# Kernel tuning notes

Hardware: AMD Instinct MI355X
Metric: run time of the kernel (lower is better)

Reference implementation:

```python
import jax, jax.numpy as jnp
import numpy as np

D_MODEL = 1024
NUM_HEADS = 16
HEAD_DIM = D_MODEL // NUM_HEADS
ROPE_THETA = 10000.0


def apply_rope(x, pos):
    # x: [B, H, S, Dh]; pos: [S] int. Interleaved-pair rotary embedding.
    d = x.shape[-1]
    inv_freq = 1.0 / (ROPE_THETA ** (jnp.arange(0, d, 2, dtype=jnp.float32) / d))  # [Dh/2]
    ang = pos.astype(jnp.float32)[:, None] * inv_freq[None, :]  # [S, Dh/2]
    cos, sin = jnp.cos(ang), jnp.sin(ang)
    x1 = x[..., 0::2]
    x2 = x[..., 1::2]
    r1 = x1 * cos - x2 * sin
    r2 = x1 * sin + x2 * cos
    return jnp.stack([r1, r2], axis=-1).reshape(x.shape)


def setup_inputs() -> dict:
    key = jax.random.key(0)
    ks = jax.random.split(key, 5)
    B, S = 4, 2048
    x = jax.random.normal(ks[0], (B, S, D_MODEL), dtype=jnp.float32)
    token_positions = jnp.arange(S, dtype=jnp.int32)
    scale = 1.0 / np.sqrt(D_MODEL)
    wq = jax.random.normal(ks[1], (D_MODEL, D_MODEL), dtype=jnp.float32) * scale
    wk = jax.random.normal(ks[2], (D_MODEL, D_MODEL), dtype=jnp.float32) * scale
    wv = jax.random.normal(ks[3], (D_MODEL, D_MODEL), dtype=jnp.float32) * scale
    wo = jax.random.normal(ks[4], (D_MODEL, D_MODEL), dtype=jnp.float32) * scale
    return {"x": x, "token_positions": token_positions, "wq": wq, "wk": wk, "wv": wv, "wo": wo}


def reference(x, token_positions, wq, wk, wv, wo):
    B, S, D = x.shape
    # Linear: einsum('d_out d_in, ... d_in -> ... d_out')
    def proj(w, t):
        return jnp.einsum('oi,bsi->bso', w, t)
    q = proj(wq, x).reshape(B, S, NUM_HEADS, HEAD_DIM).transpose(0, 2, 1, 3)  # [B,H,S,Dh]
    k = proj(wk, x).reshape(B, S, NUM_HEADS, HEAD_DIM).transpose(0, 2, 1, 3)
    v = proj(wv, x).reshape(B, S, NUM_HEADS, HEAD_DIM).transpose(0, 2, 1, 3)
    q = apply_rope(q, token_positions)
    k = apply_rope(k, token_positions)
    scores = jnp.einsum('bhqd,bhkd->bhqk', q, k) / jnp.sqrt(jnp.float32(HEAD_DIM))
    causal = jnp.tril(jnp.ones((S, S), dtype=bool))  # True = keep
    scores = jnp.where(causal, scores, -jnp.inf)
    attn = jax.nn.softmax(scores, axis=-1)
    out = jnp.einsum('bhqk,bhkd->bhqd', attn, v)  # [B,H,S,Dh]
    out = out.transpose(0, 2, 1, 3).reshape(B, S, D)
    return jnp.einsum('oi,bsi->bso', wo, out)
```

## Files before the change

### kernel.cpp

```cpp
#include <hip/hip_runtime.h>
#include <hip/hip_fp16.h>

#define DM   1024
#define NH   16
#define HD   64
#define BATCH 4
#define SEQ  2048
#define MROWS (BATCH*SEQ)
#define BHSD  ((size_t)BATCH*NH*SEQ*HD)

using f32x4 = __attribute__((ext_vector_type(4))) float;
using f16x8 = __attribute__((ext_vector_type(8))) _Float16;
using f16x4 = __attribute__((ext_vector_type(4))) _Float16;
using fp16x2 = __attribute__((ext_vector_type(2))) __fp16;
using u32x2 = __attribute__((ext_vector_type(2))) unsigned int;

__device__ __forceinline__ void gload_lds16(const void* g, void* l) {
    __builtin_amdgcn_global_load_lds(
        (const __attribute__((address_space(1))) void*)g,
        (__attribute__((address_space(3))) void*)l, 16, 0, 0);
}

__device__ __forceinline__ float red16_max(float v) {
    u32x2 r = __builtin_amdgcn_permlane16_swap(__float_as_uint(v), __float_as_uint(v), false, false);
    return fmaxf(__uint_as_float(r[0]), __uint_as_float(r[1]));
}
__device__ __forceinline__ float red32_max(float v) {
    u32x2 r = __builtin_amdgcn_permlane32_swap(__float_as_uint(v), __float_as_uint(v), false, false);
    return fmaxf(__uint_as_float(r[0]), __uint_as_float(r[1]));
}
__device__ __forceinline__ float red16_add(float v) {
    u32x2 r = __builtin_amdgcn_permlane16_swap(__float_as_uint(v), __float_as_uint(v), false, false);
    return __uint_as_float(r[0]) + __uint_as_float(r[1]);
}
__device__ __forceinline__ float red32_add(float v) {
    u32x2 r = __builtin_amdgcn_permlane32_swap(__float_as_uint(v), __float_as_uint(v), false, false);
    return __uint_as_float(r[0]) + __uint_as_float(r[1]);
}

__global__ __launch_bounds__(256) void f32_to_f16(const float* __restrict__ in,
                                                  _Float16* __restrict__ out, int n) {
    int i = (blockIdx.x * 256 + threadIdx.x) * 4;
    if (i >= n) return;
    float4 v = *(const float4*)(in + i);
    union { _Float16 h[4]; ushort4 u; } cv;
    cv.h[0] = (_Float16)v.x; cv.h[1] = (_Float16)v.y;
    cv.h[2] = (_Float16)v.z; cv.h[3] = (_Float16)v.w;
    *(ushort4*)(out + i) = cv.u;
}

__global__ __launch_bounds__(256) void rope_table(const int* __restrict__ pos,
                                                  float2* __restrict__ tab) {
    int idx = blockIdx.x * 256 + threadIdx.x;
    int s = idx >> 5, j = idx & 31;
    float p = (float)pos[s];
    float invf = powf(10000.0f, -(float)j / 32.0f);
    float ang = p * invf;
    tab[idx] = make_float2(cosf(ang), sinf(ang));
}

template<int MODE>
__global__ __launch_bounds__(256, 2)
void gemmT(const _Float16* __restrict__ A, const _Float16* __restrict__ Bw,
           float* __restrict__ outF, _Float16* __restrict__ qkv,
           const float2* __restrict__ rope) {
    constexpr int NK = DM / 32;
    __shared__ __align__(16) _Float16 ldsA[2][256][32];
    __shared__ __align__(16) _Float16 ldsB[2][128][32];
    const int tid  = threadIdx.x;
    const int lane = tid & 63;
    const int wid  = tid >> 6;
    const int m0 = blockIdx.x * 256;
    const int n0 = blockIdx.y * 128;
    const int wm = (wid >> 1) * 128;
    const int wn = (wid & 1) * 64;
    const int g   = lane >> 4;
    const int r16 = lane & 15;

    const _Float16* srcA[4];
    int dstA[4];
    #pragma unroll
    for (int L = 0; L < 4; ++L) {
        const int u = L*256 + tid, row = u >> 2, c = (u & 3) ^ ((row >> 1) & 3);
        srcA[L] = A + (size_t)(m0 + row)*DM + c*8;
        dstA[L] = u*8;
    }
    const _Float16* srcB[2];
    int dstB[2];
    #pragma unroll
    for (int L = 0; L < 2; ++L) {
        const int u = L*256 + tid, row = u >> 2, c = (u & 3) ^ ((row >> 1) & 3);
        srcB[L] = Bw + (size_t)(n0 + row)*DM + c*8;
        dstB[L] = u*8;
    }

    #define STAGE(buf, kt) do {                                        \
        const int ko = (kt)*32;                                        \
        _Float16* bA = &ldsA[(buf)][0][0];                             \
        _Float16* bB = &ldsB[(buf)][0][0];                             \
        gload_lds16(srcA[0] + ko, bA + dstA[0]);                       \
        gload_lds16(srcA[1] + ko, bA + dstA[1]);                       \
        gload_lds16(srcA[2] + ko, bA + dstA[2]);                       \
        gload_lds16(srcA[3] + ko, bA + dstA[3]);                       \
        gload_lds16(srcB[0] + ko, bB + dstB[0]);                       \
        gload_lds16(srcB[1] + ko, bB + dstB[1]);                       \
    } while (0)

    f32x4 acc[8][4] = {};

    STAGE(0, 0);
    for (int kt = 0; kt < NK; ++kt) {
        __syncthreads();
        if (kt + 1 < NK) STAGE((kt + 1) & 1, kt + 1);
        const int buf = kt & 1;
        f16x8 af[8], bf[4];
        #pragma unroll
        for (int i = 0; i < 8; ++i) {
            int row = wm + i*16 + r16;
            af[i] = *(const f16x8*)&ldsA[buf][row][(g ^ ((row >> 1) & 3)) * 8];
        }
        #pragma unroll
        for (int j = 0; j < 4; ++j) {
            int row = wn + j*16 + r16;
            bf[j] = *(const f16x8*)&ldsB[buf][row][(g ^ ((row >> 1) & 3)) * 8];
        }
        __builtin_amdgcn_s_setprio(1);
        #pragma unroll
        for (int i = 0; i < 8; ++i)
            #pragma unroll
            for (int j = 0; j < 4; ++j)
                acc[i][j] = __builtin_amdgcn_mfma_f32_16x16x32_f16(af[i], bf[j], acc[i][j], 0, 0, 0);
        __builtin_amdgcn_s_setprio(0);
    }
    #undef STAGE

    #pragma unroll
    for (int i = 0; i < 8; ++i) {
        #pragma unroll
        for (int j = 0; j < 4; ++j) {
            if constexpr (MODE == 0) {
                #pragma unroll
                for (int r = 0; r < 4; ++r) {
                    const int m = m0 + wm + i*16 + g*4 + r;
                    const int n = n0 + wn + j*16 + r16;
                    outF[(size_t)m*DM + n] = acc[i][j][r];
                }
            } else {
                const int n = n0 + wn + j*16 + r16;
                const int sel = n >> 10;
                const int cc = n & 1023;
                const int h = cc >> 6, dd = cc & 63;
                if (sel == 2) {
                    const int mb = m0 + wm + i*16 + g*4;
                    const int s0 = mb & (SEQ - 1), b = mb >> 11;
                    f16x4 pk;
                    #pragma unroll
                    for (int r = 0; r < 4; ++r) pk[r] = (_Float16)acc[i][j][r];
                    *(f16x4*)(qkv + 2*BHSD + ((size_t)((b*NH + h)*HD + dd))*SEQ + s0) = pk;
                } else {
                    #pragma unroll
                    for (int r = 0; r < 4; ++r) {
                        const int m = m0 + wm + i*16 + g*4 + r;
                        float v = acc[i][j][r];
                        float vp = __shfl_xor(v, 1);
                        const int s = m & (SEQ - 1), b = m >> 11;
                        float2 cs = rope[(s << 5) + (dd >> 1)];
                        float o;
                        if (dd & 1) o = vp * cs.y + v * cs.x;
                        else        o = v * cs.x - vp * cs.y;
                        if (sel == 0) o *= 0.18033688f;
                        qkv[(size_t)sel*BHSD + ((size_t)((b*NH + h)*SEQ + s))*HD + dd] = (_Float16)o;
                    }
                }
            }
        }
    }
}

__device__ __forceinline__ void process_tile(
    const _Float16 (*__restrict__ Klb)[64], const _Float16 (*__restrict__ Vlb)[64],
    const f16x8 (&qf)[2], f32x4 (&ot)[4], float &m, float &l,
    const int Rq, const int kv0, const int g, const int r16) {

    f32x4 sT[4] = {};
    const int kchunkBase = r16 & 7;
    __builtin_amdgcn_s_setprio(1);
    #pragma unroll
    for (int ks = 0; ks < 2; ++ks) {
        #pragma unroll
        for (int n = 0; n < 4; ++n) {
            f16x8 kf = *(const f16x8*)&Klb[n*16 + r16][(((ks<<2)|g) ^ kchunkBase)*8];
            sT[n] = __builtin_amdgcn_mfma_f32_16x16x32_f16(kf, qf[ks], sT[n], 0, 0, 0);
        }
    }
    __builtin_amdgcn_s_setprio(0);

    const bool full = (kv0 + 63 <= Rq);
    float sv[16];
    if (full) {
        #pragma unroll
        for (int n = 0; n < 4; ++n)
            #pragma unroll
            for (int r = 0; r < 4; ++r) sv[n*4 + r] = sT[n][r];
    } else {
        const int q = Rq + r16;
        #pragma unroll
        for (int n = 0; n < 4; ++n)
            #pragma unroll
            for (int r = 0; r < 4; ++r)
                sv[n*4 + r] = (kv0 + n*16 + 4*g + r <= q) ? sT[n][r] : -INFINITY;
    }
    float mx = sv[0];
    #pragma unroll
    for (int i = 1; i < 16; ++i) mx = fmaxf(mx, sv[i]);
    mx = red32_max(red16_max(mx));
    const bool need = (mx > m + 8.f);
    if (__any(need)) {
        float mnew = need ? mx : m;
        float al = exp2f(m - mnew);
        m = mnew;
        l *= al;
        #pragma unroll
        for (int n = 0; n < 4; ++n) ot[n] *= al;
    }
    float ps = 0.f;
    #pragma unroll
    for (int i = 0; i < 16; ++i) { sv[i] = exp2f(sv[i] - m); ps += sv[i]; }
    l += red32_add(red16_add(ps));

    uint pk[4][2];
    #pragma unroll
    for (int t = 0; t < 4; ++t)
        #pragma unroll
        for (int rp = 0; rp < 2; ++rp) {
            union { fp16x2 h; uint u; } cv;
            cv.h = __builtin_amdgcn_cvt_pkrtz(sv[t*4 + 2*rp], sv[t*4 + 2*rp + 1]);
            pk[t][rp] = cv.u;
        }
    uint w[2][4];
    #pragma unroll
    for (int kk = 0; kk < 2; ++kk)
        #pragma unroll
        for (int rp = 0; rp < 2; ++rp) {
            u32x2 s32 = __builtin_amdgcn_permlane32_swap(pk[2*kk][rp], pk[2*kk + 1][rp], false, false);
            u32x2 s16 = __builtin_amdgcn_permlane16_swap(s32[0], s32[1], false, false);
            w[kk][rp]     = s16[0];
            w[kk][2 + rp] = s16[1];
        }

    __builtin_amdgcn_s_setprio(1);
    #pragma unroll
    for (int ks = 0; ks < 2; ++ks) {
        union { uint u[4]; f16x8 h; } pb;
        #pragma unroll
        for (int j2 = 0; j2 < 4; ++j2) pb.u[j2] = w[ks][j2];
        #pragma unroll
        for (int n = 0; n < 4; ++n) {
            f16x8 vf = *(const f16x8*)&Vlb[n*16 + r16][(((ks<<2)|g) ^ kchunkBase)*8];
            ot[n] = __builtin_amdgcn_mfma_f32_16x16x32_f16(vf, pb.h, ot[n], 0, 0, 0);
        }
    }
    __builtin_amdgcn_s_setprio(0);
}

__global__ __launch_bounds__(256, 4)
void attn_kernel(const _Float16* __restrict__ qkv, _Float16* __restrict__ ao) {
    const int tid = threadIdx.x, lane = tid & 63, w = tid >> 6;
    const int g = lane >> 4, r16 = lane & 15;
    const int bh = blockIdx.x;
    const int jq = blockIdx.y;
    const int q0h = (31 - jq) * 64, q0l = jq * 64;
    const _Float16* Q   = qkv + (size_t)bh * SEQ * HD;
    const _Float16* Kp  = qkv + BHSD + (size_t)bh * SEQ * HD;
    const _Float16* Vpt = qkv + 2*BHSD + (size_t)bh * SEQ * HD;

    __shared__ __align__(16) _Float16 Kl[2][64][64];
    __shared__ __align__(16) _Float16 Vl[2][64][64];

    const int rA = tid >> 3,        rB = 32 + (tid >> 3);
    const int lcA = (tid & 7) ^ (rA & 7), lcB = (tid & 7) ^ (rB & 7);
    const _Float16* KsrcA = Kp  + (size_t)rA*HD + lcA*8;
    const _Float16* KsrcB = Kp  + (size_t)rB*HD + lcB*8;
    const _Float16* VsrcA = Vpt + (size_t)rA*SEQ + lcA*8;
    const _Float16* VsrcB = Vpt + (size_t)rB*SEQ + lcB*8;

    const int Rh = q0h + w*16, Rl = q0l + w*16;
    f16x8 qfh[2], qfl[2];
    #pragma unroll
    for (int ks = 0; ks < 2; ++ks) {
        qfh[ks] = *(const f16x8*)(Q + (size_t)(Rh + r16)*HD + ks*32 + g*8);
        qfl[ks] = *(const f16x8*)(Q + (size_t)(Rl + r16)*HD + ks*32 + g*8);
    }

    f32x4 oth[4] = {}, otl[4] = {};
    float mh = -INFINITY, lh = 0.f, ml_ = -INFINITY, ll_ = 0.f;

    const int nth = (q0h >> 6) + 1;
    const int ntl = (q0l >> 6) + 1;

    #define STAGE(buf, kv0) do {                                              \
        gload_lds16(KsrcA + (size_t)(kv0)*HD, &Kl[(buf)][0][0] + tid*8);      \
        gload_lds16(KsrcB + (size_t)(kv0)*HD, &Kl[(buf)][0][0] + (256+tid)*8);\
        gload_lds16(VsrcA + (kv0),            &Vl[(buf)][0][0] + tid*8);      \
        gload_lds16(VsrcB + (kv0),            &Vl[(buf)][0][0] + (256+tid)*8);\
    } while (0)

    STAGE(0, 0);
    for (int kt = 0; kt < nth; ++kt) {
        const int kv0 = kt << 6;
        __syncthreads();
        if (kt + 1 < nth) STAGE((kt + 1) & 1, (kt + 1) << 6);
        const int buf = kt & 1;

        if (kv0 <= Rh + 15)
            process_tile(Kl[buf], Vl[buf], qfh, oth, mh, lh, Rh, kv0, g, r16);
        if (kt < ntl)
            process_tile(Kl[buf], Vl[buf], qfl, otl, ml_, ll_, Rl, kv0, g, r16);
    }
    #undef STAGE

    const int b = bh >> 4, h = bh & 15;
    const float invh = 1.0f / lh, invl = 1.0f / ll_;
    _Float16* dsth = ao + ((size_t)(b*SEQ + Rh + r16))*DM + h*HD + g*4;
    _Float16* dstl = ao + ((size_t)(b*SEQ + Rl + r16))*DM + h*HD + g*4;
    #pragma unroll
    for (int n = 0; n < 4; ++n) {
        f16x4 pkh, pkl;
        #pragma unroll
        for (int r = 0; r < 4; ++r) {
            pkh[r] = (_Float16)(oth[n][r] * invh);
            pkl[r] = (_Float16)(otl[n][r] * invl);
        }
        *(f16x4*)(dsth + n*16) = pkh;
        *(f16x4*)(dstl + n*16) = pkl;
    }
}

extern "C" void kernel_launch(void* const* d_in, const int* in_sizes, int n_in,
                              void* d_out, int out_size, void* d_ws, size_t ws_size,
                              hipStream_t stream) {
    const float* x  = (const float*)d_in[0];
    const int*   tp = (const int*)d_in[1];
    const float* wq = (const float*)d_in[2];
    const float* wk = (const float*)d_in[3];
    const float* wv = (const float*)d_in[4];
    const float* wo = (const float*)d_in[5];
    float* out = (float*)d_out;

    char* ws = (char*)d_ws;
    _Float16* xh  = (_Float16*)(ws);
    _Float16* whq = (_Float16*)(ws + 16777216);
    _Float16* woh = (_Float16*)(ws + 23068672);
    _Float16* qkv = (_Float16*)(ws + 25165824);
    _Float16* ao  = (_Float16*)(ws + 75497472);
    float2*   rope= (float2*)  (ws + 92274688);

    f32_to_f16<<<MROWS*DM/1024, 256, 0, stream>>>(x, xh, MROWS*DM);
    f32_to_f16<<<DM*DM/1024, 256, 0, stream>>>(wq, whq,            DM*DM);
    f32_to_f16<<<DM*DM/1024, 256, 0, stream>>>(wk, whq + DM*DM,    DM*DM);
    f32_to_f16<<<DM*DM/1024, 256, 0, stream>>>(wv, whq + 2*DM*DM,  DM*DM);
    f32_to_f16<<<DM*DM/1024, 256, 0, stream>>>(wo, woh,            DM*DM);
    rope_table<<<SEQ*32/256, 256, 0, stream>>>(tp, rope);

    gemmT<1><<<dim3(MROWS/256, 3*DM/128), 256, 0, stream>>>(xh, whq, nullptr, qkv, rope);
    attn_kernel<<<dim3(BATCH*NH, 16), 256, 0, stream>>>(qkv, ao);
    gemmT<0><<<dim3(MROWS/256, DM/128), 256, 0, stream>>>(ao, woh, out, nullptr, nullptr);
}
```

Before: 215.9 us.

## Restructure projection GEMMs with 512-thread blocks, triple-buffered LDS and grid swizzle

Replaces the double-buffered 256-thread GEMM with a 512-thread, 8-wave kernel that prefetches three K-tiles ahead. Waits use explicit vmcnt counts and raw barriers instead of __syncthreads. The QKV projection now uses 256x256 tiles, and block indices are remapped so neighbouring blocks share A/B tiles in L2. This aims to hide global-load latency better and raise data reuse, at the cost of more LDS per block (one block per CU) and fragile hand-counted waitcnt logic.

```diff
diff --git a/kernel.cpp b/kernel.cpp
--- a/kernel.cpp
+++ b/kernel.cpp
@@ -60,36 +60,45 @@
 }
 
 template<int MODE>
-__global__ __launch_bounds__(256, 2)
-void gemmT(const _Float16* __restrict__ A, const _Float16* __restrict__ Bw,
+__global__ __launch_bounds__(512, 1)
+void gemmP(const _Float16* __restrict__ A, const _Float16* __restrict__ Bw,
            float* __restrict__ outF, _Float16* __restrict__ qkv,
            const float2* __restrict__ rope) {
     constexpr int NK = DM / 32;
-    __shared__ __align__(16) _Float16 ldsA[2][256][32];
-    __shared__ __align__(16) _Float16 ldsB[2][128][32];
+    constexpr int BN = MODE ? 256 : 128;
+    constexpr int WTM = MODE ? 8 : 4;
+    constexpr int BL = MODE ? 2 : 1;
+    __shared__ __align__(16) _Float16 ldsA[3][256][32];
+    __shared__ __align__(16) _Float16 ldsB[3][BN][32];
+
     const int tid  = threadIdx.x;
     const int lane = tid & 63;
     const int wid  = tid >> 6;
-    const int m0 = blockIdx.x * 256;
-    const int n0 = blockIdx.y * 128;
-    const int wm = (wid >> 1) * 128;
-    const int wn = (wid & 1) * 64;
+
+    const int nwg  = gridDim.x * gridDim.y;
+    const int flat = blockIdx.y * gridDim.x + blockIdx.x;
+    const int swz  = (flat % 8) * (nwg >> 3) + (flat >> 3);
+    const int m0 = (swz % gridDim.x) * 256;
+    const int n0 = (swz / gridDim.x) * BN;
+
+    const int wm = MODE ? ((wid >> 2) * 128) : ((wid >> 1) * 64);
+    const int wn = MODE ? ((wid & 3) * 64)   : ((wid & 1) * 64);
     const int g   = lane >> 4;
     const int r16 = lane & 15;
 
-    const _Float16* srcA[4];
-    int dstA[4];
-    #pragma unroll
-    for (int L = 0; L < 4; ++L) {
-        const int u = L*256 + tid, row = u >> 2, c = (u & 3) ^ ((row >> 1) & 3);
+    const _Float16* srcA[2];
+    int dstA[2];
+    #pragma unroll
+    for (int L = 0; L < 2; ++L) {
+        const int u = L*512 + tid, row = u >> 2, c = (u & 3) ^ ((row >> 1) & 3);
         srcA[L] = A + (size_t)(m0 + row)*DM + c*8;
         dstA[L] = u*8;
     }
-    const _Float16* srcB[2];
-    int dstB[2];
-    #pragma unroll
-    for (int L = 0; L < 2; ++L) {
-        const int u = L*256 + tid, row = u >> 2, c = (u & 3) ^ ((row >> 1) & 3);
+    const _Float16* srcB[BL];
+    int dstB[BL];
+    #pragma unroll
+    for (int L = 0; L < BL; ++L) {
+        const int u = L*512 + tid, row = u >> 2, c = (u & 3) ^ ((row >> 1) & 3);
         srcB[L] = Bw + (size_t)(n0 + row)*DM + c*8;
         dstB[L] = u*8;
     }
@@ -100,22 +109,24 @@
         _Float16* bB = &ldsB[(buf)][0][0];                             \
         gload_lds16(srcA[0] + ko, bA + dstA[0]);                       \
         gload_lds16(srcA[1] + ko, bA + dstA[1]);                       \
-        gload_lds16(srcA[2] + ko, bA + dstA[2]);                       \
-        gload_lds16(srcA[3] + ko, bA + dstA[3]);                       \
         gload_lds16(srcB[0] + ko, bB + dstB[0]);                       \
-        gload_lds16(srcB[1] + ko, bB + dstB[1]);                       \
+        if constexpr (BL == 2) gload_lds16(srcB[1] + ko, bB + dstB[1]);\
     } while (0)
 
-    f32x4 acc[8][4] = {};
+    f32x4 acc[WTM][4] = {};
 
     STAGE(0, 0);
-    for (int kt = 0; kt < NK; ++kt) {
-        __syncthreads();
-        if (kt + 1 < NK) STAGE((kt + 1) & 1, kt + 1);
-        const int buf = kt & 1;
-        f16x8 af[8], bf[4];
-        #pragma unroll
-        for (int i = 0; i < 8; ++i) {
+    STAGE(1, 1);
+    STAGE(2, 2);
+    if constexpr (MODE == 1) asm volatile("s_waitcnt vmcnt(8)" ::: "memory");
+    else                     asm volatile("s_waitcnt vmcnt(6)" ::: "memory");
+    __builtin_amdgcn_s_barrier();
+
+    int buf = 0;
+    for (int t = 0; t < NK; ++t) {
+        f16x8 af[WTM], bf[4];
+        #pragma unroll
+        for (int i = 0; i < WTM; ++i) {
             int row = wm + i*16 + r16;
             af[i] = *(const f16x8*)&ldsA[buf][row][(g ^ ((row >> 1) & 3)) * 8];
         }
@@ -124,18 +135,34 @@
             int row = wn + j*16 + r16;
             bf[j] = *(const f16x8*)&ldsB[buf][row][(g ^ ((row >> 1) & 3)) * 8];
         }
+        asm volatile("s_waitcnt lgkmcnt(0)" ::: "memory");
+        __builtin_amdgcn_sched_barrier(0);
+        __builtin_amdgcn_s_barrier();
+        if (t + 3 < NK) STAGE(buf, t + 3);
         __builtin_amdgcn_s_setprio(1);
         #pragma unroll
-        for (int i = 0; i < 8; ++i)
+        for (int i = 0; i < WTM; ++i)
             #pragma unroll
             for (int j = 0; j < 4; ++j)
                 acc[i][j] = __builtin_amdgcn_mfma_f32_16x16x32_f16(af[i], bf[j], acc[i][j], 0, 0, 0);
         __builtin_amdgcn_s_setprio(0);
+        if constexpr (MODE == 1) {
+            if (t + 3 < NK)      asm volatile("s_waitcnt vmcnt(8)" ::: "memory");
+            else if (t + 2 < NK) asm volatile("s_waitcnt vmcnt(4)" ::: "memory");
+            else if (t + 1 < NK) asm volatile("s_waitcnt vmcnt(0)" ::: "memory");
+        } else {
+            if (t + 3 < NK)      asm volatile("s_waitcnt vmcnt(6)" ::: "memory");
+            else if (t + 2 < NK) asm volatile("s_waitcnt vmcnt(3)" ::: "memory");
+            else if (t + 1 < NK) asm volatile("s_waitcnt vmcnt(0)" ::: "memory");
+        }
+        __builtin_amdgcn_sched_barrier(0);
+        __builtin_amdgcn_s_barrier();
+        buf = (buf == 2) ? 0 : buf + 1;
     }
     #undef STAGE
 
     #pragma unroll
-    for (int i = 0; i < 8; ++i) {
+    for (int i = 0; i < WTM; ++i) {
         #pragma unroll
         for (int j = 0; j < 4; ++j) {
             if constexpr (MODE == 0) {
@@ -362,7 +389,7 @@
     f32_to_f16<<<DM*DM/1024, 256, 0, stream>>>(wo, woh,            DM*DM);
     rope_table<<<SEQ*32/256, 256, 0, stream>>>(tp, rope);
 
-    gemmT<1><<<dim3(MROWS/256, 3*DM/128), 256, 0, stream>>>(xh, whq, nullptr, qkv, rope);
+    gemmP<1><<<dim3(MROWS/256, 3*DM/256), 512, 0, stream>>>(xh, whq, nullptr, qkv, rope);
     attn_kernel<<<dim3(BATCH*NH, 16), 256, 0, stream>>>(qkv, ao);
-    gemmT<0><<<dim3(MROWS/256, DM/128), 256, 0, stream>>>(ao, woh, out, nullptr, nullptr);
-}
+    gemmP<0><<<dim3(MROWS/256, DM/128), 512, 0, stream>>>(ao, woh, out, nullptr, nullptr);
+}
```

Measured after the change: 223.2 us. 1.03x slower.
